# Kernel optimization log

Hardware: AMD Instinct MI355X
Metric: run time of the kernel (lower is better)

Reference implementation:

```python
import jax, jax.numpy as jnp
import numpy as np
from functools import partial

RED = 128      # reduced_dim
MK = 24        # r2d_m * r2d_k
HD, WD = 32, 16  # depth feature grid after 3 stride-2 convs on 256x128


def _conv(x, w, b):
    # torch Conv2d(k=3, stride=2, padding=1), NCHW / OIHW
    y = jax.lax.conv_general_dilated(
        x, w, window_strides=(2, 2), padding=((1, 1), (1, 1)),
        dimension_numbers=("NCHW", "OIHW", "NCHW"))
    return y + b[None, :, None, None]


def setup_inputs() -> dict:
    key = jax.random.key(0)
    ks = jax.random.split(key, 24)
    B = 64
    s = 0.02
    inp = {
        "features": jax.random.normal(ks[0], (B, 129, 768), jnp.float32),
        "d": jax.random.uniform(ks[1], (B, 1, 256, 128), jnp.float32),
        "W_rg": jax.random.normal(ks[2], (768, RED), jnp.float32) * s,
        "b_rg": jnp.zeros((RED,), jnp.float32),
        "W_rl": jax.random.normal(ks[3], (768, RED), jnp.float32) * s,
        "b_rl": jnp.zeros((RED,), jnp.float32),
        "conv1_w": jax.random.normal(ks[4], (64, 1, 3, 3), jnp.float32) * s,
        "conv1_b": jnp.zeros((64,), jnp.float32),
        "conv2_w": jax.random.normal(ks[5], (128, 64, 3, 3), jnp.float32) * s,
        "conv2_b": jnp.zeros((128,), jnp.float32),
        "conv3_w": jax.random.normal(ks[6], (128, 128, 3, 3), jnp.float32) * s,
        "conv3_b": jnp.zeros((128,), jnp.float32),
        "g_depth": jax.random.normal(ks[7], (RED,), jnp.float32),
        "W_merge": jax.random.normal(ks[8], (2 * RED, RED), jnp.float32) * s,
        "b_merge": jnp.zeros((RED,), jnp.float32),
        "W_q": jax.random.normal(ks[9], (2 * RED, RED), jnp.float32) * s,
        "b_q": jnp.zeros((RED,), jnp.float32),
        "W_v": jax.random.normal(ks[10], (RED, RED), jnp.float32) * s,
        "b_v": jnp.zeros((RED,), jnp.float32),
        "W_sel": jax.random.normal(ks[11], (RED, 3 * MK), jnp.float32) * s,
        "b_sel": jnp.zeros((3 * MK,), jnp.float32),
        "W_cls": jax.random.normal(ks[12], (RED, 751), jnp.float32) * s,
    }
    return inp


def _forward(features, d, W_rg, b_rg, W_rl, b_rl, conv1_w, conv1_b, conv2_w,
             conv2_b, conv3_w, conv3_b, g_depth, W_merge, b_merge, W_q, b_q,
             W_v, b_v, W_sel, b_sel, W_cls):
    B = features.shape[0]
    N = features.shape[1] - 1
    global_feat = features[:, 0] @ W_rg + b_rg                 # (B, 128)
    local_feat = features[:, 1:] @ W_rl + b_rl                 # (B, N, 128)
    lcg = jnp.concatenate(
        [jnp.broadcast_to(global_feat[:, None], (B, N, RED)), local_feat], -1)

    dep = _conv(_conv(_conv(d, conv1_w, conv1_b), conv2_w, conv2_b),
                conv3_w, conv3_b)                              # (B,128,32,16)
    dep = dep.transpose(0, 2, 3, 1).reshape(B, HD * WD, RED)
    lcgd = jnp.concatenate(
        [jnp.broadcast_to(g_depth[None, None], (B, HD * WD, RED)), dep], -1)
    lcgd = lcgd @ W_merge + b_merge

    q = lcg @ W_q + b_q                                        # (B,N,128)
    v = lcgd @ W_v + b_v                                       # (B,512,128)
    sel = jax.nn.sigmoid(q @ W_sel + b_sel)                    # (B,N,72)
    lx = sel[:, :, 0:2 * MK:2]                                 # (B,N,24)
    ly = sel[:, :, 1:2 * MK:2]
    attn = jax.nn.softmax(sel[:, :, 2 * MK:], axis=-1)

    # integer corner grid (original uses // stride == floor(loc*(dim-1)))
    x1 = jnp.floor(lx * (WD - 1))
    x2 = jnp.minimum(x1 + 1.0, float(WD - 1))
    y1 = jnp.floor(ly * (HD - 1))
    y2 = jnp.minimum(y1 + 1.0, float(HD - 1))
    xi1, xi2 = x1.astype(jnp.int32), x2.astype(jnp.int32)
    yi1, yi2 = y1.astype(jnp.int32), y2.astype(jnp.int32)

    # faithful to original gather: index = x_idx * Wd + y_idx
    gather = jax.vmap(lambda vb, ib: vb[ib])                   # (512,C),(N,K)->(N,K,C)
    f0 = gather(v, xi1 * WD + yi2)
    f1 = gather(v, xi2 * WD + yi2)
    f2 = gather(v, xi2 * WD + yi1)
    f3 = gather(v, xi1 * WD + yi1)

    # query coordinates scaled by full grid size (as in the original)
    x = lx * WD
    y = ly * HD
    w_ = x2 - x1
    h_ = y2 - y1
    degenerate = (h_ == 0) | (w_ == 0)
    denom = jnp.where(h_ * w_ == 0, 1.0, h_ * w_)
    coeff = jnp.where(degenerate, 2.0, 1.0 / denom)            # (B,N,24)
    xv0 = jnp.where(w_ == 0, 1.0, x2 - x)
    xv1 = jnp.where(w_ == 0, 1.0, x - x1)
    yv0 = jnp.where(h_ == 0, 1.0, y2 - y)
    yv1 = jnp.where(h_ == 0, 1.0, y - y1)

    # xv^T @ [[f0,f1],[f2,f3]] @ yv, per channel
    interp = coeff[..., None] * (
        xv0[..., None] * (f0 * yv0[..., None] + f1 * yv1[..., None]) +
        xv1[..., None] * (f2 * yv0[..., None] + f3 * yv1[..., None]))

    r2d_feat = jnp.mean(interp * attn[..., None], axis=-2)     # (B,N,128)
    final_embedding = jnp.mean(r2d_feat, axis=1)               # (B,128)
    cls_score = final_embedding @ W_cls                        # (B,751)
    return cls_score, final_embedding


def reference(features, d, W_rg, b_rg, W_rl, b_rl, conv1_w, conv1_b, conv2_w,
              conv2_b, conv3_w, conv3_b, g_depth, W_merge, b_merge, W_q, b_q,
              W_v, b_v, W_sel, b_sel, W_cls):
    return _forward(features, d, W_rg, b_rg, W_rl, b_rl, conv1_w, conv1_b,
                    conv2_w, conv2_b, conv3_w, conv3_b, g_depth, W_merge,
                    b_merge, W_q, b_q, W_v, b_v, W_sel, b_sel, W_cls)
```

## Files before the change

### kernel.cpp

```cpp
#include <hip/hip_runtime.h>
#include <hip/hip_bf16.h>


typedef __attribute__((ext_vector_type(8))) short short8;
typedef __attribute__((ext_vector_type(4))) short shortx4;
typedef __attribute__((ext_vector_type(4))) float floatx4;

__global__ __launch_bounds__(256) void prep1_k(
    const float* __restrict__ W_q, const float* __restrict__ W_sel,
    const float* __restrict__ W_merge, const float* __restrict__ W_v,
    const float* __restrict__ g_depth, const float* __restrict__ b_merge,
    const float* __restrict__ features, const float* __restrict__ W_rg,
    const float* __restrict__ b_rg,
    float* __restrict__ W_qs, float* __restrict__ W_mv,
    float* __restrict__ c0, float* __restrict__ gfeat)
{
    int bid = blockIdx.x, t = threadIdx.x;
    if (bid < 72) {
        int j = bid;
        float acc = 0.f;
        for (int k = 0; k < 128; ++k)
            acc = fmaf(W_q[t * 128 + k], W_sel[k * 72 + j], acc);
        W_qs[t * 72 + j] = acc;
    } else if (bid < 200) {
        int j = bid - 72;
        if (t < 128) {
            float acc = 0.f;
            for (int k = 0; k < 128; ++k)
                acc = fmaf(W_merge[(128 + t) * 128 + k], W_v[k * 128 + j], acc);
            W_mv[t * 128 + j] = acc;
        }
    } else if (bid == 200) {
        if (t < 128) {
            float acc = b_merge[t];
            for (int k = 0; k < 128; ++k)
                acc = fmaf(g_depth[k], W_merge[k * 128 + t], acc);
            c0[t] = acc;
        }
    } else {
        int j = bid - 201;
        if (t < 64) {
            float acc = b_rg[j];
            const float* fr = features + (long)t * 129 * 768;
            for (int k = 0; k < 768; ++k)
                acc = fmaf(fr[k], W_rg[k * 128 + j], acc);
            gfeat[t * 128 + j] = acc;
        }
    }
}

__global__ __launch_bounds__(256) void prep2_k(
    const float* __restrict__ W_rl, const float* __restrict__ W_qs,
    const float* __restrict__ W_sel, const float* __restrict__ b_rl,
    const float* __restrict__ b_q, const float* __restrict__ b_sel,
    const float* __restrict__ gfeat, const float* __restrict__ c0,
    const float* __restrict__ W_v, const float* __restrict__ b_v,
    float* __restrict__ W_big, float* __restrict__ rowbias,
    float* __restrict__ c0v)
{
    int bid = blockIdx.x, t = threadIdx.x;
    if (bid < 216) {
        int j = bid / 3;
        int i = (bid % 3) * 256 + t;
        float acc = 0.f;
        for (int k = 0; k < 128; ++k)
            acc = fmaf(W_rl[i * 128 + k], W_qs[(128 + k) * 72 + j], acc);
        W_big[i * 72 + j] = acc;
    } else if (bid < 288) {
        int j = bid - 216;
        if (t < 64) {
            float vb = b_sel[j];
            for (int k = 0; k < 128; ++k) {
                vb = fmaf(b_rl[k], W_qs[(128 + k) * 72 + j], vb);
                vb = fmaf(b_q[k], W_sel[k * 72 + j], vb);
            }
            float acc = vb;
            for (int k = 0; k < 128; ++k)
                acc = fmaf(gfeat[t * 128 + k], W_qs[k * 72 + j], acc);
            rowbias[t * 72 + j] = acc;
        }
    } else {
        if (t < 128) {
            float acc = b_v[t];
            for (int k = 0; k < 128; ++k)
                acc = fmaf(c0[k], W_v[k * 128 + t], acc);
            c0v[t] = acc;
        }
    }
}

__global__ __launch_bounds__(256) void prep3_k(
    const float* __restrict__ W_mv,
    __hip_bfloat16* __restrict__ Bh, __hip_bfloat16* __restrict__ Bl)
{
    int idx = blockIdx.x * 256 + threadIdx.x;
    int n = idx >> 7, k = idx & 127;
    float w = W_mv[k * 128 + n];
    __hip_bfloat16 h = __float2bfloat16(w);
    Bh[idx] = h;
    Bl[idx] = __float2bfloat16(w - __bfloat162float(h));
}

__global__ __launch_bounds__(256) void prep4_k(
    const float* __restrict__ W_big,
    __hip_bfloat16* __restrict__ Wbh, __hip_bfloat16* __restrict__ Wbl)
{
    int idx = blockIdx.x * 256 + threadIdx.x;
    if (idx >= 80 * 768) return;
    int n = idx / 768, k = idx - n * 768;
    float w = (n < 72) ? W_big[k * 72 + n] : 0.f;
    __hip_bfloat16 h = __float2bfloat16(w);
    Wbh[idx] = h;
    Wbl[idx] = __float2bfloat16(w - __bfloat162float(h));
}

__global__ __launch_bounds__(256) void wt2_k(const float* __restrict__ w,
                                             __hip_bfloat16* __restrict__ wt)
{
    int idx = blockIdx.x * 256 + threadIdx.x;
    if (idx >= 128 * 576) return;
    int oc = idx / 576, k = idx % 576;
    int s = k >> 6, ic = k & 63;
    wt[idx] = __float2bfloat16(w[oc * 576 + ic * 9 + s]);
}
__global__ __launch_bounds__(256) void wt3_k(const float* __restrict__ w,
                                             __hip_bfloat16* __restrict__ wt)
{
    int idx = blockIdx.x * 256 + threadIdx.x;
    if (idx >= 128 * 1152) return;
    int oc = idx / 1152, k = idx % 1152;
    int s = k >> 7, ic = k & 127;
    wt[idx] = __float2bfloat16(w[oc * 1152 + ic * 9 + s]);
}

__global__ __launch_bounds__(256) void conv1_k(
    const float* __restrict__ d, const float* __restrict__ w,
    const float* __restrict__ bias, __hip_bfloat16* __restrict__ out)
{
    __shared__ float in_s[3][66];
    __shared__ float ws_[576];
    __shared__ float bs_[64];
    int tid = threadIdx.x;
    int owhalf = blockIdx.x & 1;
    int oh = (blockIdx.x >> 1) & 127;
    int b  = blockIdx.x >> 8;
    int owbase = owhalf * 32;

    for (int l = tid; l < 576; l += 256) ws_[l] = w[l];
    if (tid < 64) bs_[tid] = bias[tid];
    for (int l = tid; l < 3 * 66; l += 256) {
        int r = l / 66, c = l % 66;
        int ih = 2 * oh - 1 + r;
        int iw = 2 * owbase - 1 + c;
        float v = 0.f;
        if ((unsigned)ih < 256u && (unsigned)iw < 128u)
            v = d[(b * 256 + ih) * 128 + iw];
        in_s[r][c] = v;
    }
    __syncthreads();

    int owl = tid >> 3, ocg = tid & 7;
    float in9[9];
#pragma unroll
    for (int r = 0; r < 3; ++r)
#pragma unroll
        for (int c = 0; c < 3; ++c)
            in9[r * 3 + c] = in_s[r][2 * owl + c];

    short8 res;
#pragma unroll
    for (int j = 0; j < 8; ++j) {
        int oc = ocg * 8 + j;
        float a = bs_[oc];
#pragma unroll
        for (int s = 0; s < 9; ++s) a = fmaf(in9[s], ws_[oc * 9 + s], a);
        union { __hip_bfloat16 h; short s; } u;
        u.h = __float2bfloat16(a);
        res[j] = u.s;
    }
    long pos = ((long)(b * 128 + oh) * 64 + owbase + owl);
    *(short8*)((short*)out + pos * 64 + ocg * 8) = res;
}

__global__ __launch_bounds__(256) void conv2_mfma(
    const __hip_bfloat16* __restrict__ in, const __hip_bfloat16* __restrict__ w2t,
    const float* __restrict__ bias, __hip_bfloat16* __restrict__ out)
{
    __shared__ short A_lds[64][32];
    __shared__ short B_lds[128][32];
    int tid = threadIdx.x;
    int oh0 = blockIdx.x * 2;
    int b   = blockIdx.y;
    int lane = tid & 63, wave = tid >> 6;
    int wr = wave >> 1, wc = wave & 1;
    floatx4 acc[2][4] = {};

    int ar = tid >> 2, aseg = tid & 3;
    int aohl = ar >> 5, aow = ar & 31;
    int boc = tid >> 2, bseg = tid & 3;

    const short* inp  = (const short*)in;
    const short* w2p  = (const short*)w2t;

    for (int s = 0; s < 9; ++s) {
        int kh = s / 3, kw = s % 3;
        int ih = 2 * (oh0 + aohl) - 1 + kh;
        int iw = 2 * aow - 1 + kw;
        bool inb = ((unsigned)ih < 128u) & ((unsigned)iw < 64u);
        const short* asrc = inp + (((b * 128 + ih) * 64 + iw) * 64 + aseg * 8);
#pragma unroll
        for (int half = 0; half < 2; ++half) {
            int koff = s * 64 + half * 32;
            short8 av = {0,0,0,0,0,0,0,0};
            if (inb) av = *(const short8*)(asrc + half * 32);
            short8 bv0 = *(const short8*)(w2p + boc * 576 + koff + bseg * 8);
            short8 bv1 = *(const short8*)(w2p + (boc + 64) * 576 + koff + bseg * 8);
            __syncthreads();
            *(short8*)&A_lds[ar][aseg * 8] = av;
            *(short8*)&B_lds[boc][bseg * 8] = bv0;
            *(short8*)&B_lds[boc + 64][bseg * 8] = bv1;
            __syncthreads();
            short8 a0 = *(const short8*)&A_lds[wr * 32 + (lane & 15)][(lane >> 4) * 8];
            short8 a1 = *(const short8*)&A_lds[wr * 32 + 16 + (lane & 15)][(lane >> 4) * 8];
#pragma unroll
            for (int ni = 0; ni < 4; ++ni) {
                short8 bv = *(const short8*)&B_lds[wc * 64 + ni * 16 + (lane & 15)][(lane >> 4) * 8];
                acc[0][ni] = __builtin_amdgcn_mfma_f32_16x16x32_bf16(a0, bv, acc[0][ni], 0, 0, 0);
                acc[1][ni] = __builtin_amdgcn_mfma_f32_16x16x32_bf16(a1, bv, acc[1][ni], 0, 0, 0);
            }
        }
    }
    float bf[4];
#pragma unroll
    for (int ni = 0; ni < 4; ++ni) bf[ni] = bias[wc * 64 + ni * 16 + (lane & 15)];
#pragma unroll
    for (int mi = 0; mi < 2; ++mi)
#pragma unroll
        for (int r = 0; r < 4; ++r) {
            int m = wr * 32 + mi * 16 + (lane >> 4) * 4 + r;
            int ohl = m >> 5, ow = m & 31;
            __hip_bfloat16* op = out + (((long)(b * 64 + oh0 + ohl) * 32) + ow) * 128;
#pragma unroll
            for (int ni = 0; ni < 4; ++ni) {
                int oc = wc * 64 + ni * 16 + (lane & 15);
                op[oc] = __float2bfloat16(acc[mi][ni][r] + bf[ni]);
            }
        }
}

__global__ __launch_bounds__(256) void conv3_mfma(
    const __hip_bfloat16* __restrict__ in, const __hip_bfloat16* __restrict__ w3t,
    const float* __restrict__ bias, float* __restrict__ dep)
{
    __shared__ short A_lds[64][32];
    __shared__ short B_lds[128][32];
    int tid = threadIdx.x;
    int oh0 = blockIdx.x * 4;
    int b   = blockIdx.y;
    int lane = tid & 63, wave = tid >> 6;
    int wr = wave >> 1, wc = wave & 1;
    floatx4 acc[2][4] = {};

    int ar = tid >> 2, aseg = tid & 3;
    int aohl = ar >> 4, aow = ar & 15;
    int boc = tid >> 2, bseg = tid & 3;

    const short* inp = (const short*)in;
    const short* w3p = (const short*)w3t;

    for (int s = 0; s < 9; ++s) {
        int kh = s / 3, kw = s % 3;
        int ih = 2 * (oh0 + aohl) - 1 + kh;
        int iw = 2 * aow - 1 + kw;
        bool inb = ((unsigned)ih < 64u) & ((unsigned)iw < 32u);
        const short* asrc = inp + (((b * 64 + ih) * 32 + iw) * 128 + aseg * 8);
#pragma unroll
        for (int q = 0; q < 4; ++q) {
            int koff = s * 128 + q * 32;
            short8 av = {0,0,0,0,0,0,0,0};
            if (inb) av = *(const short8*)(asrc + q * 32);
            short8 bv0 = *(const short8*)(w3p + boc * 1152 + koff + bseg * 8);
            short8 bv1 = *(const short8*)(w3p + (boc + 64) * 1152 + koff + bseg * 8);
            __syncthreads();
            *(short8*)&A_lds[ar][aseg * 8] = av;
            *(short8*)&B_lds[boc][bseg * 8] = bv0;
            *(short8*)&B_lds[boc + 64][bseg * 8] = bv1;
            __syncthreads();
            short8 a0 = *(const short8*)&A_lds[wr * 32 + (lane & 15)][(lane >> 4) * 8];
            short8 a1 = *(const short8*)&A_lds[wr * 32 + 16 + (lane & 15)][(lane >> 4) * 8];
#pragma unroll
            for (int ni = 0; ni < 4; ++ni) {
                short8 bv = *(const short8*)&B_lds[wc * 64 + ni * 16 + (lane & 15)][(lane >> 4) * 8];
                acc[0][ni] = __builtin_amdgcn_mfma_f32_16x16x32_bf16(a0, bv, acc[0][ni], 0, 0, 0);
                acc[1][ni] = __builtin_amdgcn_mfma_f32_16x16x32_bf16(a1, bv, acc[1][ni], 0, 0, 0);
            }
        }
    }
    float bf[4];
#pragma unroll
    for (int ni = 0; ni < 4; ++ni) bf[ni] = bias[wc * 64 + ni * 16 + (lane & 15)];
#pragma unroll
    for (int mi = 0; mi < 2; ++mi)
#pragma unroll
        for (int r = 0; r < 4; ++r) {
            int m = wr * 32 + mi * 16 + (lane >> 4) * 4 + r;
            float* op = dep + ((long)b * 512 + oh0 * 16 + m) * 128;
#pragma unroll
            for (int ni = 0; ni < 4; ++ni) {
                int oc = wc * 64 + ni * 16 + (lane & 15);
                op[oc] = acc[mi][ni][r] + bf[ni];
            }
        }
}

__global__ __launch_bounds__(256) void vgemm_mfma(
    const float* __restrict__ dep, const __hip_bfloat16* __restrict__ Bh,
    const __hip_bfloat16* __restrict__ Bl, const float* __restrict__ c0v,
    float* __restrict__ v)
{
    __shared__ short Ah[64][136];
    __shared__ short Al[64][136];
    int tid = threadIdx.x;
    int m0 = blockIdx.x * 64;

    for (int l4 = tid; l4 < 64 * 32; l4 += 256) {
        int r = l4 >> 5, c4 = l4 & 31;
        const float* sp = dep + ((long)(m0 + r) << 7) + c4 * 4;
        shortx4 hv, lv;
#pragma unroll
        for (int i = 0; i < 4; ++i) {
            float f = sp[i];
            union { __hip_bfloat16 b; short s; } uh, ul;
            uh.b = __float2bfloat16(f);
            ul.b = __float2bfloat16(f - __bfloat162float(uh.b));
            hv[i] = uh.s; lv[i] = ul.s;
        }
        *(shortx4*)&Ah[r][c4 * 4] = hv;
        *(shortx4*)&Al[r][c4 * 4] = lv;
    }
    __syncthreads();

    int lane = tid & 63, wave = tid >> 6;
    int wr = wave >> 1, wc = wave & 1;
    int l16 = lane & 15, lh = lane >> 4;
    floatx4 acc[2][4] = {};
#pragma unroll
    for (int kk = 0; kk < 4; ++kk) {
        short8 ah[2], al[2];
#pragma unroll
        for (int mi = 0; mi < 2; ++mi) {
            ah[mi] = *(const short8*)&Ah[wr * 32 + mi * 16 + l16][kk * 32 + lh * 8];
            al[mi] = *(const short8*)&Al[wr * 32 + mi * 16 + l16][kk * 32 + lh * 8];
        }
#pragma unroll
        for (int nf = 0; nf < 4; ++nf) {
            int gn = wc * 64 + nf * 16 + l16;
            short8 bh = *(const short8*)((const short*)Bh + gn * 128 + kk * 32 + lh * 8);
            short8 bl = *(const short8*)((const short*)Bl + gn * 128 + kk * 32 + lh * 8);
#pragma unroll
            for (int mi = 0; mi < 2; ++mi) {
                acc[mi][nf] = __builtin_amdgcn_mfma_f32_16x16x32_bf16(ah[mi], bh, acc[mi][nf], 0, 0, 0);
                acc[mi][nf] = __builtin_amdgcn_mfma_f32_16x16x32_bf16(al[mi], bh, acc[mi][nf], 0, 0, 0);
                acc[mi][nf] = __builtin_amdgcn_mfma_f32_16x16x32_bf16(ah[mi], bl, acc[mi][nf], 0, 0, 0);
            }
        }
    }
#pragma unroll
    for (int nf = 0; nf < 4; ++nf) {
        int gn = wc * 64 + nf * 16 + l16;
        float cv = c0v[gn];
#pragma unroll
        for (int mi = 0; mi < 2; ++mi)
#pragma unroll
            for (int r = 0; r < 4; ++r) {
                int m = m0 + wr * 32 + mi * 16 + lh * 4 + r;
                v[(long)m * 128 + gn] = acc[mi][nf][r] + cv;
            }
    }
}

__global__ __launch_bounds__(256) void selmfma_k(
    const float* __restrict__ F, const __hip_bfloat16* __restrict__ Wbh,
    const __hip_bfloat16* __restrict__ Wbl, const float* __restrict__ rowbias,
    float* __restrict__ lx, float* __restrict__ ly, float* __restrict__ attn)
{
    __shared__ short Ah[16][136];
    __shared__ short Al[16][136];
    int tid = threadIdx.x;
    int m0 = blockIdx.x * 16;
    int padd = (m0 >> 7) + 1;
    int lane = tid & 63, wave = tid >> 6;
    int l16 = lane & 15, lh = lane >> 4;

    int sr = tid >> 4, sc = (tid & 15) * 8;
    const float* fsrc = F + (long)(m0 + sr + padd) * 768 + sc;

    floatx4 acc0 = {0.f, 0.f, 0.f, 0.f};
    floatx4 acc1 = {0.f, 0.f, 0.f, 0.f};
    bool two = (wave == 3);
    const short* bhp = (const short*)Wbh;
    const short* blp = (const short*)Wbl;
    int gn0 = wave * 16 + l16;
    int gn1 = 64 + l16;

    for (int c = 0; c < 6; ++c) {
        __syncthreads();
        float4 f0 = *(const float4*)(fsrc + c * 128);
        float4 f1 = *(const float4*)(fsrc + c * 128 + 4);
        shortx4 h0, l0, h1, l1;
#pragma unroll
        for (int i = 0; i < 4; ++i) {
            union { __hip_bfloat16 b; short s; } uh, ul;
            float fa = (&f0.x)[i];
            uh.b = __float2bfloat16(fa);
            ul.b = __float2bfloat16(fa - __bfloat162float(uh.b));
            h0[i] = uh.s; l0[i] = ul.s;
            float fb = (&f1.x)[i];
            uh.b = __float2bfloat16(fb);
            ul.b = __float2bfloat16(fb - __bfloat162float(uh.b));
            h1[i] = uh.s; l1[i] = ul.s;
        }
        *(shortx4*)&Ah[sr][sc]     = h0;
        *(shortx4*)&Ah[sr][sc + 4] = h1;
        *(shortx4*)&Al[sr][sc]     = l0;
        *(shortx4*)&Al[sr][sc + 4] = l1;
        __syncthreads();
#pragma unroll
        for (int ks = 0; ks < 4; ++ks) {
            short8 ah = *(const short8*)&Ah[l16][ks * 32 + lh * 8];
            short8 al = *(const short8*)&Al[l16][ks * 32 + lh * 8];
            int koff = c * 128 + ks * 32 + lh * 8;
            short8 bh0 = *(const short8*)(bhp + gn0 * 768 + koff);
            short8 bl0 = *(const short8*)(blp + gn0 * 768 + koff);
            acc0 = __builtin_amdgcn_mfma_f32_16x16x32_bf16(ah, bh0, acc0, 0, 0, 0);
            acc0 = __builtin_amdgcn_mfma_f32_16x16x32_bf16(al, bh0, acc0, 0, 0, 0);
            acc0 = __builtin_amdgcn_mfma_f32_16x16x32_bf16(ah, bl0, acc0, 0, 0, 0);
            if (two) {
                short8 bh1 = *(const short8*)(bhp + gn1 * 768 + koff);
                short8 bl1 = *(const short8*)(blp + gn1 * 768 + koff);
                acc1 = __builtin_amdgcn_mfma_f32_16x16x32_bf16(ah, bh1, acc1, 0, 0, 0);
                acc1 = __builtin_amdgcn_mfma_f32_16x16x32_bf16(al, bh1, acc1, 0, 0, 0);
                acc1 = __builtin_amdgcn_mfma_f32_16x16x32_bf16(ah, bl1, acc1, 0, 0, 0);
            }
        }
    }

    if (wave < 3) {
        int j = wave * 16 + l16;
#pragma unroll
        for (int r = 0; r < 4; ++r) {
            int row = m0 + lh * 4 + r;
            float val = acc0[r] + rowbias[(row >> 7) * 72 + j];
            float sg = 1.f / (1.f + expf(-val));
            if (j & 1) ly[row * 24 + (j >> 1)] = sg;
            else       lx[row * 24 + (j >> 1)] = sg;
        }
    } else {
#pragma unroll
        for (int r = 0; r < 4; ++r) {
            int row = m0 + lh * 4 + r;
            int b72 = (row >> 7) * 72;
            float s0 = 1.f / (1.f + expf(-(acc0[r] + rowbias[b72 + 48 + l16])));
            float s1 = -1e30f;
            if (l16 < 8)
                s1 = 1.f / (1.f + expf(-(acc1[r] + rowbias[b72 + 64 + l16])));
            float mx = fmaxf(s0, s1);
#pragma unroll
            for (int s = 1; s < 16; s <<= 1)
                mx = fmaxf(mx, __shfl_xor(mx, s));
            float e0 = expf(s0 - mx);
            float e1 = (l16 < 8) ? expf(s1 - mx) : 0.f;
            float sum = e0 + e1;
#pragma unroll
            for (int s = 1; s < 16; s <<= 1)
                sum += __shfl_xor(sum, s);
            attn[row * 24 + l16] = e0 / sum;
            if (l16 < 8) attn[row * 24 + 16 + l16] = e1 / sum;
        }
    }
}

__global__ __launch_bounds__(128) void r2d_k(
    const float* __restrict__ v, const float* __restrict__ lx,
    const float* __restrict__ ly, const float* __restrict__ attn,
    float* __restrict__ r2d)
{
    int n = blockIdx.x;
    int b = blockIdx.y;
    int c = threadIdx.x;
    int row = b * 128 + n;
    __shared__ float sx[24], sy[24], sa[24];
    if (c < 24) { sx[c] = lx[row * 24 + c]; sy[c] = ly[row * 24 + c]; sa[c] = attn[row * 24 + c]; }
    __syncthreads();
    const float* vb = v + (long)b * 512 * 128;
    float acc = 0.f;
    for (int k = 0; k < 24; ++k) {
        float lxv = sx[k], lyv = sy[k], a = sa[k];
        float x1 = floorf(lxv * 15.f), x2 = fminf(x1 + 1.f, 15.f);
        float y1 = floorf(lyv * 31.f), y2 = fminf(y1 + 1.f, 31.f);
        int xi1 = (int)x1, xi2 = (int)x2, yi1 = (int)y1, yi2 = (int)y2;
        float f0 = vb[(xi1 * 16 + yi2) * 128 + c];
        float f1 = vb[(xi2 * 16 + yi2) * 128 + c];
        float f2 = vb[(xi2 * 16 + yi1) * 128 + c];
        float f3 = vb[(xi1 * 16 + yi1) * 128 + c];
        float x = lxv * 16.f, y = lyv * 32.f;
        float w_ = x2 - x1, h_ = y2 - y1;
        float hwp = h_ * w_;
        bool deg = (h_ == 0.f) || (w_ == 0.f);
        float denom = (hwp == 0.f) ? 1.f : hwp;
        float coeff = deg ? 2.f : 1.f / denom;
        float xv0 = (w_ == 0.f) ? 1.f : (x2 - x);
        float xv1 = (w_ == 0.f) ? 1.f : (x - x1);
        float yv0 = (h_ == 0.f) ? 1.f : (y2 - y);
        float yv1 = (h_ == 0.f) ? 1.f : (y - y1);
        float interp = coeff * (xv0 * (f0 * yv0 + f1 * yv1) + xv1 * (f2 * yv0 + f3 * yv1));
        acc = fmaf(interp, a, acc);
    }
    r2d[(long)row * 128 + c] = acc * (1.f / 24.f);
}

__global__ __launch_bounds__(128) void fe_k(const float* __restrict__ r2d,
                                            float* __restrict__ fe)
{
    int b = blockIdx.x;
    int c = threadIdx.x;
    float acc = 0.f;
    for (int nn = 0; nn < 128; ++nn) acc += r2d[((long)b * 128 + nn) * 128 + c];
    fe[b * 128 + c] = acc * (1.f / 128.f);
}

__global__ __launch_bounds__(256) void cls_k(
    const float* __restrict__ fe, const float* __restrict__ W_cls,
    float* __restrict__ out)
{
    int idx = blockIdx.x * 256 + threadIdx.x;
    if (idx >= 64 * 751) return;
    int m = idx / 751, n = idx - m * 751;
    const float* fr = fe + m * 128;
    float acc = 0.f;
    for (int k = 0; k < 128; ++k)
        acc = fmaf(fr[k], W_cls[k * 751 + n], acc);
    out[idx] = acc;
}

extern "C" void kernel_launch(void* const* d_in, const int* in_sizes, int n_in,
                              void* d_out, int out_size, void* d_ws, size_t ws_size,
                              hipStream_t stream)
{
    const float* features = (const float*)d_in[0];
    const float* d        = (const float*)d_in[1];
    const float* W_rg  = (const float*)d_in[2];
    const float* b_rg  = (const float*)d_in[3];
    const float* W_rl  = (const float*)d_in[4];
    const float* b_rl  = (const float*)d_in[5];
    const float* c1w   = (const float*)d_in[6];
    const float* c1b   = (const float*)d_in[7];
    const float* c2w   = (const float*)d_in[8];
    const float* c2b   = (const float*)d_in[9];
    const float* c3w   = (const float*)d_in[10];
    const float* c3b   = (const float*)d_in[11];
    const float* g_depth = (const float*)d_in[12];
    const float* W_merge = (const float*)d_in[13];
    const float* b_merge = (const float*)d_in[14];
    const float* W_q   = (const float*)d_in[15];
    const float* b_q   = (const float*)d_in[16];
    const float* W_v   = (const float*)d_in[17];
    const float* b_v   = (const float*)d_in[18];
    const float* W_sel = (const float*)d_in[19];
    const float* b_sel = (const float*)d_in[20];
    const float* W_cls = (const float*)d_in[21];
    float* out = (float*)d_out;

    char* ws = (char*)d_ws;
    __hip_bfloat16* c1 = (__hip_bfloat16*)(ws + 0);
    float* dep    = (float*)(ws + 0);
    float* v      = (float*)(ws + 33554432);
    __hip_bfloat16* c2 = (__hip_bfloat16*)(ws + 67108864);
    __hip_bfloat16* w2t = (__hip_bfloat16*)(ws + 100663296);
    __hip_bfloat16* w3t = (__hip_bfloat16*)(ws + 100810752);
    float* W_qs    = (float*)(ws + 101105664);
    float* W_mv    = (float*)(ws + 101179392);
    float* W_big   = (float*)(ws + 101244928);
    float* rowbias = (float*)(ws + 101466112);
    float* c0b     = (float*)(ws + 101484544);
    float* c0v     = (float*)(ws + 101485056);
    float* gfeat   = (float*)(ws + 101485568);
    __hip_bfloat16* Wmv_bh = (__hip_bfloat16*)(ws + 101518336);
    __hip_bfloat16* Wmv_bl = (__hip_bfloat16*)(ws + 101551104);
    __hip_bfloat16* Wbig_h = (__hip_bfloat16*)(ws + 101583872);
    __hip_bfloat16* Wbig_l = (__hip_bfloat16*)(ws + 101706752);
    float* lxb    = (float*)(ws + 111411200);
    float* lyb    = (float*)(ws + 112197632);
    float* attnb  = (float*)(ws + 112984064);
    float* r2d    = (float*)(ws + 113836544);

    float* fe = out + 64 * 751;

    prep1_k<<<329, 256, 0, stream>>>(W_q, W_sel, W_merge, W_v, g_depth, b_merge,
                                     features, W_rg, b_rg, W_qs, W_mv, c0b, gfeat);
    prep2_k<<<289, 256, 0, stream>>>(W_rl, W_qs, W_sel, b_rl, b_q, b_sel,
                                     gfeat, c0b, W_v, b_v, W_big, rowbias, c0v);
    prep3_k<<<64, 256, 0, stream>>>(W_mv, Wmv_bh, Wmv_bl);
    prep4_k<<<240, 256, 0, stream>>>(W_big, Wbig_h, Wbig_l);
    wt2_k<<<288, 256, 0, stream>>>(c2w, w2t);
    wt3_k<<<576, 256, 0, stream>>>(c3w, w3t);

    conv1_k<<<16384, 256, 0, stream>>>(d, c1w, c1b, c1);
    conv2_mfma<<<dim3(32, 64), 256, 0, stream>>>(c1, w2t, c2b, c2);
    conv3_mfma<<<dim3(8, 64), 256, 0, stream>>>(c2, w3t, c3b, dep);

    vgemm_mfma<<<512, 256, 0, stream>>>(dep, Wmv_bh, Wmv_bl, c0v, v);
    selmfma_k<<<512, 256, 0, stream>>>(features, Wbig_h, Wbig_l, rowbias,
                                       lxb, lyb, attnb);

    r2d_k<<<dim3(128, 64), 128, 0, stream>>>(v, lxb, lyb, attnb, r2d);
    fe_k<<<64, 128, 0, stream>>>(r2d, fe);
    cls_k<<<188, 256, 0, stream>>>(fe, W_cls, out);
}
```

Before: 240.3 us.

## Stage conv input halo tile in LDS once and read weights directly

conv2 and conv3 now load the full input halo tile (5 rows of padded width, all channels) into shared memory once per block, then build MFMA A fragments straight from that tile for every 3x3 tap. Weight fragments are read from global memory (cache) instead of being staged through LDS. This removes the two barriers per K-step and the repeated global reads of overlapping input windows. conv3 also shrinks to 2 output rows per block with one M fragment per wave and launches twice as many blocks. The cost is uncoalesced per-lane weight loads and larger LDS use, which may limit occupancy.

```diff
diff --git a/kernel.cpp b/kernel.cpp
--- a/kernel.cpp
+++ b/kernel.cpp
@@ -5,6 +5,8 @@
 typedef __attribute__((ext_vector_type(8))) short short8;
 typedef __attribute__((ext_vector_type(4))) short shortx4;
 typedef __attribute__((ext_vector_type(4))) float floatx4;
+
+#define MFMA16(a, b, c) __builtin_amdgcn_mfma_f32_16x16x32_bf16(a, b, c, 0, 0, 0)
 
 __global__ __launch_bounds__(256) void prep1_k(
     const float* __restrict__ W_q, const float* __restrict__ W_sel,
@@ -186,63 +188,67 @@
     const __hip_bfloat16* __restrict__ in, const __hip_bfloat16* __restrict__ w2t,
     const float* __restrict__ bias, __hip_bfloat16* __restrict__ out)
 {
-    __shared__ short A_lds[64][32];
-    __shared__ short B_lds[128][32];
+    __shared__ short ins[5][66][68];
     int tid = threadIdx.x;
     int oh0 = blockIdx.x * 2;
     int b   = blockIdx.y;
+    const short* inp = (const short*)in;
+    int ih0 = 2 * oh0 - 1;
+
+    for (int l = tid; l < 330 * 8; l += 256) {
+        int seg = l & 7, pos = l >> 3;
+        int rr = pos / 66, cc = pos - rr * 66;
+        int ih = ih0 + rr, iw = cc - 1;
+        short8 v = {0,0,0,0,0,0,0,0};
+        if ((unsigned)ih < 128u && (unsigned)iw < 64u)
+            v = *(const short8*)(inp + ((((long)b * 128 + ih) * 64 + iw) * 64 + seg * 8));
+        *(short8*)&ins[rr][cc][seg * 8] = v;
+    }
+    __syncthreads();
+
     int lane = tid & 63, wave = tid >> 6;
     int wr = wave >> 1, wc = wave & 1;
+    int l16 = lane & 15, lh = lane >> 4;
     floatx4 acc[2][4] = {};
-
-    int ar = tid >> 2, aseg = tid & 3;
-    int aohl = ar >> 5, aow = ar & 31;
-    int boc = tid >> 2, bseg = tid & 3;
-
-    const short* inp  = (const short*)in;
-    const short* w2p  = (const short*)w2t;
-
-    for (int s = 0; s < 9; ++s) {
-        int kh = s / 3, kw = s % 3;
-        int ih = 2 * (oh0 + aohl) - 1 + kh;
-        int iw = 2 * aow - 1 + kw;
-        bool inb = ((unsigned)ih < 128u) & ((unsigned)iw < 64u);
-        const short* asrc = inp + (((b * 128 + ih) * 64 + iw) * 64 + aseg * 8);
-#pragma unroll
-        for (int half = 0; half < 2; ++half) {
-            int koff = s * 64 + half * 32;
-            short8 av = {0,0,0,0,0,0,0,0};
-            if (inb) av = *(const short8*)(asrc + half * 32);
-            short8 bv0 = *(const short8*)(w2p + boc * 576 + koff + bseg * 8);
-            short8 bv1 = *(const short8*)(w2p + (boc + 64) * 576 + koff + bseg * 8);
-            __syncthreads();
-            *(short8*)&A_lds[ar][aseg * 8] = av;
-            *(short8*)&B_lds[boc][bseg * 8] = bv0;
-            *(short8*)&B_lds[boc + 64][bseg * 8] = bv1;
-            __syncthreads();
-            short8 a0 = *(const short8*)&A_lds[wr * 32 + (lane & 15)][(lane >> 4) * 8];
-            short8 a1 = *(const short8*)&A_lds[wr * 32 + 16 + (lane & 15)][(lane >> 4) * 8];
-#pragma unroll
-            for (int ni = 0; ni < 4; ++ni) {
-                short8 bv = *(const short8*)&B_lds[wc * 64 + ni * 16 + (lane & 15)][(lane >> 4) * 8];
-                acc[0][ni] = __builtin_amdgcn_mfma_f32_16x16x32_bf16(a0, bv, acc[0][ni], 0, 0, 0);
-                acc[1][ni] = __builtin_amdgcn_mfma_f32_16x16x32_bf16(a1, bv, acc[1][ni], 0, 0, 0);
+    const short* w2p = (const short*)w2t;
+
+    int pos0 = wr * 32 + l16;
+    int pos1 = pos0 + 16;
+    int oa0 = pos0 >> 5, ow0 = pos0 & 31;
+    int oa1 = pos1 >> 5, ow1 = pos1 & 31;
+
+#pragma unroll
+    for (int kh = 0; kh < 3; ++kh)
+#pragma unroll
+        for (int kw = 0; kw < 3; ++kw) {
+#pragma unroll
+            for (int half = 0; half < 2; ++half) {
+                short8 a0 = *(const short8*)&ins[2 * oa0 + kh][2 * ow0 + kw][half * 32 + lh * 8];
+                short8 a1 = *(const short8*)&ins[2 * oa1 + kh][2 * ow1 + kw][half * 32 + lh * 8];
+                int koff = (kh * 3 + kw) * 64 + half * 32 + lh * 8;
+#pragma unroll
+                for (int ni = 0; ni < 4; ++ni) {
+                    int gn = wc * 64 + ni * 16 + l16;
+                    short8 bv = *(const short8*)(w2p + gn * 576 + koff);
+                    acc[0][ni] = MFMA16(a0, bv, acc[0][ni]);
+                    acc[1][ni] = MFMA16(a1, bv, acc[1][ni]);
+                }
             }
         }
-    }
+
     float bf[4];
 #pragma unroll
-    for (int ni = 0; ni < 4; ++ni) bf[ni] = bias[wc * 64 + ni * 16 + (lane & 15)];
+    for (int ni = 0; ni < 4; ++ni) bf[ni] = bias[wc * 64 + ni * 16 + l16];
 #pragma unroll
     for (int mi = 0; mi < 2; ++mi)
 #pragma unroll
         for (int r = 0; r < 4; ++r) {
-            int m = wr * 32 + mi * 16 + (lane >> 4) * 4 + r;
+            int m = wr * 32 + mi * 16 + lh * 4 + r;
             int ohl = m >> 5, ow = m & 31;
             __hip_bfloat16* op = out + (((long)(b * 64 + oh0 + ohl) * 32) + ow) * 128;
 #pragma unroll
             for (int ni = 0; ni < 4; ++ni) {
-                int oc = wc * 64 + ni * 16 + (lane & 15);
+                int oc = wc * 64 + ni * 16 + l16;
                 op[oc] = __float2bfloat16(acc[mi][ni][r] + bf[ni]);
             }
         }
@@ -252,65 +258,64 @@
     const __hip_bfloat16* __restrict__ in, const __hip_bfloat16* __restrict__ w3t,
     const float* __restrict__ bias, float* __restrict__ dep)
 {
-    __shared__ short A_lds[64][32];
-    __shared__ short B_lds[128][32];
+    __shared__ short ins[5][34][132];
     int tid = threadIdx.x;
-    int oh0 = blockIdx.x * 4;
+    int oh0 = blockIdx.x * 2;
     int b   = blockIdx.y;
+    const short* inp = (const short*)in;
+    int ih0 = 2 * oh0 - 1;
+
+    for (int l = tid; l < 170 * 16; l += 256) {
+        int seg = l & 15, pos = l >> 4;
+        int rr = pos / 34, cc = pos - rr * 34;
+        int ih = ih0 + rr, iw = cc - 1;
+        short8 v = {0,0,0,0,0,0,0,0};
+        if ((unsigned)ih < 64u && (unsigned)iw < 32u)
+            v = *(const short8*)(inp + ((((long)b * 64 + ih) * 32 + iw) * 128 + seg * 8));
+        *(short8*)&ins[rr][cc][seg * 8] = v;
+    }
+    __syncthreads();
+
     int lane = tid & 63, wave = tid >> 6;
     int wr = wave >> 1, wc = wave & 1;
-    floatx4 acc[2][4] = {};
-
-    int ar = tid >> 2, aseg = tid & 3;
-    int aohl = ar >> 4, aow = ar & 15;
-    int boc = tid >> 2, bseg = tid & 3;
-
-    const short* inp = (const short*)in;
+    int l16 = lane & 15, lh = lane >> 4;
+    floatx4 acc[4] = {};
     const short* w3p = (const short*)w3t;
 
-    for (int s = 0; s < 9; ++s) {
-        int kh = s / 3, kw = s % 3;
-        int ih = 2 * (oh0 + aohl) - 1 + kh;
-        int iw = 2 * aow - 1 + kw;
-        bool inb = ((unsigned)ih < 64u) & ((unsigned)iw < 32u);
-        const short* asrc = inp + (((b * 64 + ih) * 32 + iw) * 128 + aseg * 8);
-#pragma unroll
-        for (int q = 0; q < 4; ++q) {
-            int koff = s * 128 + q * 32;
-            short8 av = {0,0,0,0,0,0,0,0};
-            if (inb) av = *(const short8*)(asrc + q * 32);
-            short8 bv0 = *(const short8*)(w3p + boc * 1152 + koff + bseg * 8);
-            short8 bv1 = *(const short8*)(w3p + (boc + 64) * 1152 + koff + bseg * 8);
-            __syncthreads();
-            *(short8*)&A_lds[ar][aseg * 8] = av;
-            *(short8*)&B_lds[boc][bseg * 8] = bv0;
-            *(short8*)&B_lds[boc + 64][bseg * 8] = bv1;
-            __syncthreads();
-            short8 a0 = *(const short8*)&A_lds[wr * 32 + (lane & 15)][(lane >> 4) * 8];
-            short8 a1 = *(const short8*)&A_lds[wr * 32 + 16 + (lane & 15)][(lane >> 4) * 8];
-#pragma unroll
-            for (int ni = 0; ni < 4; ++ni) {
-                short8 bv = *(const short8*)&B_lds[wc * 64 + ni * 16 + (lane & 15)][(lane >> 4) * 8];
-                acc[0][ni] = __builtin_amdgcn_mfma_f32_16x16x32_bf16(a0, bv, acc[0][ni], 0, 0, 0);
-                acc[1][ni] = __builtin_amdgcn_mfma_f32_16x16x32_bf16(a1, bv, acc[1][ni], 0, 0, 0);
+    int pos = wr * 16 + l16;
+    int oa = pos >> 4, ow = pos & 15;
+
+#pragma unroll
+    for (int kh = 0; kh < 3; ++kh)
+#pragma unroll
+        for (int kw = 0; kw < 3; ++kw) {
+#pragma unroll
+            for (int ks = 0; ks < 4; ++ks) {
+                short8 a = *(const short8*)&ins[2 * oa + kh][2 * ow + kw][ks * 32 + lh * 8];
+                int koff = (kh * 3 + kw) * 128 + ks * 32 + lh * 8;
+#pragma unroll
+                for (int ni = 0; ni < 4; ++ni) {
+                    int gn = wc * 64 + ni * 16 + l16;
+                    short8 bv = *(const short8*)(w3p + gn * 1152 + koff);
+                    acc[ni] = MFMA16(a, bv, acc[ni]);
+                }
             }
         }
-    }
+
     float bf[4];
 #pragma unroll
-    for (int ni = 0; ni < 4; ++ni) bf[ni] = bias[wc * 64 + ni * 16 + (lane & 15)];
-#pragma unroll
-    for (int mi = 0; mi < 2; ++mi)
-#pragma unroll
-        for (int r = 0; r < 4; ++r) {
-            int m = wr * 32 + mi * 16 + (lane >> 4) * 4 + r;
-            float* op = dep + ((long)b * 512 + oh0 * 16 + m) * 128;
-#pragma unroll
-            for (int ni = 0; ni < 4; ++ni) {
-                int oc = wc * 64 + ni * 16 + (lane & 15);
-                op[oc] = acc[mi][ni][r] + bf[ni];
-            }
-        }
+    for (int ni = 0; ni < 4; ++ni) bf[ni] = bias[wc * 64 + ni * 16 + l16];
+#pragma unroll
+    for (int r = 0; r < 4; ++r) {
+        int m = wr * 16 + lh * 4 + r;
+        int oa2 = m >> 4, ow2 = m & 15;
+        float* op = dep + ((long)b * 512 + (oh0 + oa2) * 16 + ow2) * 128;
+#pragma unroll
+        for (int ni = 0; ni < 4; ++ni) {
+            int oc = wc * 64 + ni * 16 + l16;
+            op[oc] = acc[ni][r] + bf[ni];
+        }
+    }
 }
 
 __global__ __launch_bounds__(256) void vgemm_mfma(
@@ -359,9 +364,9 @@
             short8 bl = *(const short8*)((const short*)Bl + gn * 128 + kk * 32 + lh * 8);
 #pragma unroll
             for (int mi = 0; mi < 2; ++mi) {
-                acc[mi][nf] = __builtin_amdgcn_mfma_f32_16x16x32_bf16(ah[mi], bh, acc[mi][nf], 0, 0, 0);
-                acc[mi][nf] = __builtin_amdgcn_mfma_f32_16x16x32_bf16(al[mi], bh, acc[mi][nf], 0, 0, 0);
-                acc[mi][nf] = __builtin_amdgcn_mfma_f32_16x16x32_bf16(ah[mi], bl, acc[mi][nf], 0, 0, 0);
+                acc[mi][nf] = MFMA16(ah[mi], bh, acc[mi][nf]);
+                acc[mi][nf] = MFMA16(al[mi], bh, acc[mi][nf]);
+                acc[mi][nf] = MFMA16(ah[mi], bl, acc[mi][nf]);
             }
         }
     }
@@ -432,15 +437,15 @@
             int koff = c * 128 + ks * 32 + lh * 8;
             short8 bh0 = *(const short8*)(bhp + gn0 * 768 + koff);
             short8 bl0 = *(const short8*)(blp + gn0 * 768 + koff);
-            acc0 = __builtin_amdgcn_mfma_f32_16x16x32_bf16(ah, bh0, acc0, 0, 0, 0);
-            acc0 = __builtin_amdgcn_mfma_f32_16x16x32_bf16(al, bh0, acc0, 0, 0, 0);
-            acc0 = __builtin_amdgcn_mfma_f32_16x16x32_bf16(ah, bl0, acc0, 0, 0, 0);
+            acc0 = MFMA16(ah, bh0, acc0);
+            acc0 = MFMA16(al, bh0, acc0);
+            acc0 = MFMA16(ah, bl0, acc0);
             if (two) {
                 short8 bh1 = *(const short8*)(bhp + gn1 * 768 + koff);
                 short8 bl1 = *(const short8*)(blp + gn1 * 768 + koff);
-                acc1 = __builtin_amdgcn_mfma_f32_16x16x32_bf16(ah, bh1, acc1, 0, 0, 0);
-                acc1 = __builtin_amdgcn_mfma_f32_16x16x32_bf16(al, bh1, acc1, 0, 0, 0);
-                acc1 = __builtin_amdgcn_mfma_f32_16x16x32_bf16(ah, bl1, acc1, 0, 0, 0);
+                acc1 = MFMA16(ah, bh1, acc1);
+                acc1 = MFMA16(al, bh1, acc1);
+                acc1 = MFMA16(ah, bl1, acc1);
             }
         }
     }
@@ -607,7 +612,7 @@
 
     conv1_k<<<16384, 256, 0, stream>>>(d, c1w, c1b, c1);
     conv2_mfma<<<dim3(32, 64), 256, 0, stream>>>(c1, w2t, c2b, c2);
-    conv3_mfma<<<dim3(8, 64), 256, 0, stream>>>(c2, w3t, c3b, dep);
+    conv3_mfma<<<dim3(16, 64), 256, 0, stream>>>(c2, w3t, c3b, dep);
 
     vgemm_mfma<<<512, 256, 0, stream>>>(dep, Wmv_bh, Wmv_bl, c0v, v);
     selmfma_k<<<512, 256, 0, stream>>>(features, Wbig_h, Wbig_l, rowbias,
```

Measured after the change: 342.3 us. 42.5% more time.
